# Kernel tuning notes

Measured on AMD Instinct MI355X. Metric: run time of the kernel, lower is better.

The kernel has to match this reference:

```python
import jax, jax.numpy as jnp
import numpy as np

N_NODES = 50000
N_EDGES = 800000
IN_CH = 256
OUT_CH = 64
HEADS = 4
NEG_SLOPE = 0.2


def setup_inputs() -> dict:
    key = jax.random.key(0)
    k = jax.random.split(key, 7)
    x = jax.random.normal(k[0], (N_NODES, IN_CH), dtype=jnp.float32)
    edge_index = jax.random.randint(k[1], (2, N_EDGES), 0, N_NODES, dtype=jnp.int32)
    # Glorot-style init for the linear projection and attention vectors
    W = jax.random.normal(k[2], (IN_CH, HEADS * OUT_CH), dtype=jnp.float32) / np.sqrt(IN_CH)
    att_src = jax.random.normal(k[3], (HEADS, OUT_CH), dtype=jnp.float32) / np.sqrt(OUT_CH)
    att_dst = jax.random.normal(k[4], (HEADS, OUT_CH), dtype=jnp.float32) / np.sqrt(OUT_CH)
    bias = jnp.zeros((HEADS * OUT_CH,), dtype=jnp.float32)
    return {"x": x, "edge_index": edge_index, "W": W,
            "att_src": att_src, "att_dst": att_dst, "bias": bias}


def reference(x, edge_index, W, att_src, att_dst, bias):
    N = x.shape[0]
    # PyG GATConv default: add self-loops
    loop = jnp.arange(N, dtype=edge_index.dtype)
    src = jnp.concatenate([edge_index[0], loop])
    dst = jnp.concatenate([edge_index[1], loop])

    h = (x @ W).reshape(N, HEADS, OUT_CH)          # [N,H,C]
    a_src = jnp.einsum('nhc,hc->nh', h, att_src)    # [N,H]
    a_dst = jnp.einsum('nhc,hc->nh', h, att_dst)    # [N,H]

    alpha = a_src[src] + a_dst[dst]                 # [E,H]
    alpha = jax.nn.leaky_relu(alpha, NEG_SLOPE)

    # segment softmax over edges grouped by destination node
    amax = jax.ops.segment_max(alpha, dst, num_segments=N)
    amax = jnp.where(jnp.isfinite(amax), amax, 0.0)
    e = jnp.exp(alpha - amax[dst])
    denom = jax.ops.segment_sum(e, dst, num_segments=N)
    coef = e / (denom[dst] + 1e-16)                 # [E,H]

    msg = coef[..., None] * h[src]                  # [E,H,C]
    out = jax.ops.segment_sum(msg, dst, num_segments=N)  # [N,H,C]
    out = out.reshape(N, HEADS * OUT_CH) + bias
    return jax.nn.relu(out)
```

## Files before the change

### kernel.cpp

```cpp
#include <hip/hip_runtime.h>
#include <hip/hip_bf16.h>

#define HC 256
#define NEG_SLOPE 0.2f
#define BM 64
#define LDKF 264

typedef short short8_t __attribute__((ext_vector_type(8)));
typedef float float4_t __attribute__((ext_vector_type(4)));
typedef int   int4_t   __attribute__((ext_vector_type(4)));

__device__ __forceinline__ unsigned short f2bf(float f) {
  unsigned u = __float_as_uint(f);
  return (unsigned short)((u + 0x7fffu + ((u >> 16) & 1u)) >> 16);
}
__device__ __forceinline__ float bf2f(unsigned short b) {
  return __uint_as_float(((unsigned)b) << 16);
}

__global__ __launch_bounds__(256) void wq_kernel(
    const float* __restrict__ W, unsigned short* __restrict__ Wq,
    int* __restrict__ deg, int n)
{
  const int f = blockIdx.x * 256 + threadIdx.x;
  if (f < 8192) {
    const int wv    = f >> 11;
    const int nt    = (f >> 9) & 3;
    const int kstep = (f >> 6) & 7;
    const int l     = f & 63;
    const int ncol  = 64 * wv + 16 * nt + (l & 15);
    const int k0    = kstep * 32 + (l >> 4) * 8;
    unsigned pk[4];
    #pragma unroll
    for (int i = 0; i < 4; ++i) {
      __hip_bfloat162 b2 = __float22bfloat162_rn(make_float2(
          W[(k0 + 2 * i) * 256 + ncol], W[(k0 + 2 * i + 1) * 256 + ncol]));
      pk[i] = *(unsigned*)&b2;
    }
    *(uint4*)&Wq[(size_t)f * 8] = make_uint4(pk[0], pk[1], pk[2], pk[3]);
  }
  if (f < n) deg[f] = 0;
}

__global__ __launch_bounds__(256) void gemm_deg(
    const float* __restrict__ x, const unsigned short* __restrict__ Wq,
    const float* __restrict__ att_src, const float* __restrict__ att_dst,
    unsigned short* __restrict__ h, float* __restrict__ a_src,
    float* __restrict__ a_dst, int nnodes,
    const int* __restrict__ ei, int* __restrict__ deg, int E, int NG, int ND)
{
  __shared__ unsigned short As[BM * LDKF];
  const int t = threadIdx.x;

  if (blockIdx.x >= NG) {
    const int b = blockIdx.x - NG;
    for (int e = b * 256 + t; e < E; e += ND * 256)
      atomicAdd(&deg[ei[E + e]], 1);
    return;
  }

  const int wv   = t >> 6;
  const int lane = t & 63;
  const int r0   = blockIdx.x * BM;

  {
    const int row = t >> 2, kcb = (t & 3) * 16;
    const int gr = r0 + row;
    #pragma unroll
    for (int k0 = 0; k0 < 256; k0 += 64) {
      float4 xv[4];
      if (gr < nnodes) {
        const float4* p = (const float4*)(x + (size_t)gr * 256 + k0 + kcb);
        xv[0] = p[0]; xv[1] = p[1]; xv[2] = p[2]; xv[3] = p[3];
      } else {
        xv[0] = xv[1] = xv[2] = xv[3] = make_float4(0.f, 0.f, 0.f, 0.f);
      }
      const float* f = (const float*)xv;
      unsigned pk[8];
      #pragma unroll
      for (int i = 0; i < 8; ++i) {
        __hip_bfloat162 b2 = __float22bfloat162_rn(make_float2(f[2 * i], f[2 * i + 1]));
        pk[i] = *(unsigned*)&b2;
      }
      uint4* d = (uint4*)&As[row * LDKF + k0 + kcb];
      d[0] = make_uint4(pk[0], pk[1], pk[2], pk[3]);
      d[1] = make_uint4(pk[4], pk[5], pk[6], pk[7]);
    }
  }
  __syncthreads();

  const int l15 = lane & 15, q = lane >> 4;
  float4_t acc[4][4] = {};

  const unsigned short* __restrict__ Bq = Wq + (size_t)wv * 16384 + lane * 8;

  #pragma unroll
  for (int kstep = 0; kstep < 8; ++kstep) {
    const int ko = kstep * 32;
    short8_t bfr[4], af[4];
    #pragma unroll
    for (int nt = 0; nt < 4; ++nt)
      bfr[nt] = *(const short8_t*)(Bq + nt * 4096 + kstep * 512);
    #pragma unroll
    for (int mt = 0; mt < 4; ++mt)
      af[mt] = *(const short8_t*)&As[(16 * mt + l15) * LDKF + ko + q * 8];
    #pragma unroll
    for (int mt = 0; mt < 4; ++mt)
      #pragma unroll
      for (int nt = 0; nt < 4; ++nt)
        acc[mt][nt] = __builtin_amdgcn_mfma_f32_16x16x32_bf16(
            bfr[nt], af[mt], acc[mt][nt], 0, 0, 0);
  }

  float4 as4[4], ad4[4];
  #pragma unroll
  for (int nt = 0; nt < 4; ++nt) {
    as4[nt] = *(const float4*)&att_src[64 * wv + 16 * nt + 4 * q];
    ad4[nt] = *(const float4*)&att_dst[64 * wv + 16 * nt + 4 * q];
  }

  #pragma unroll
  for (int mt = 0; mt < 4; ++mt) {
    const int node = r0 + 16 * mt + l15;
    const bool ok = node < nnodes;
    float ps = 0.f, pd = 0.f;
    #pragma unroll
    for (int nt = 0; nt < 4; ++nt) {
      const float4_t v = acc[mt][nt];
      if (ok) {
        __hip_bfloat162 b01 = __float22bfloat162_rn(make_float2(v[0], v[1]));
        __hip_bfloat162 b23 = __float22bfloat162_rn(make_float2(v[2], v[3]));
        uint2 u = make_uint2(*(unsigned*)&b01, *(unsigned*)&b23);
        *(uint2*)&h[(size_t)node * 256 + 64 * wv + 16 * nt + 4 * q] = u;
      }
      ps += v[0] * as4[nt].x + v[1] * as4[nt].y + v[2] * as4[nt].z + v[3] * as4[nt].w;
      pd += v[0] * ad4[nt].x + v[1] * ad4[nt].y + v[2] * ad4[nt].z + v[3] * ad4[nt].w;
    }
    ps += __shfl_down(ps, 16); ps += __shfl_down(ps, 32);
    pd += __shfl_down(pd, 16); pd += __shfl_down(pd, 32);
    if (ok && lane < 16) {
      a_src[node * 4 + wv] = ps;
      a_dst[node * 4 + wv] = pd;
    }
  }
}

__global__ __launch_bounds__(256) void scan_p1(const int* __restrict__ deg,
                                               int* __restrict__ bsum, int n)
{
  __shared__ int ws[4];
  const int t = threadIdx.x, lane = t & 63, wv = t >> 6;
  const int base = blockIdx.x * 1024 + t * 4;
  int4 v = make_int4(0, 0, 0, 0);
  if (base + 3 < n) v = *(const int4*)&deg[base];
  else {
    if (base + 0 < n) v.x = deg[base + 0];
    if (base + 1 < n) v.y = deg[base + 1];
    if (base + 2 < n) v.z = deg[base + 2];
  }
  int s = (v.x + v.y) + (v.z + v.w);
  #pragma unroll
  for (int off = 32; off; off >>= 1) s += __shfl_down(s, off, 64);
  if (lane == 0) ws[wv] = s;
  __syncthreads();
  if (t == 0) bsum[blockIdx.x] = (ws[0] + ws[1]) + (ws[2] + ws[3]);
}

__global__ __launch_bounds__(1024) void scan_p2(const int* __restrict__ bsum,
                                                int* __restrict__ boff,
                                                int* __restrict__ rowptr,
                                                int nb, int n)
{
  __shared__ int wsum[16], woff[16];
  const int t = threadIdx.x, lane = t & 63, wv = t >> 6;
  int v = (t < nb) ? bsum[t] : 0;
  int sc = v;
  #pragma unroll
  for (int off = 1; off < 64; off <<= 1) {
    int u = __shfl_up(sc, off, 64);
    if (lane >= off) sc += u;
  }
  if (lane == 63) wsum[wv] = sc;
  __syncthreads();
  if (t == 0) {
    int run = 0;
    #pragma unroll
    for (int i = 0; i < 16; ++i) { int x = wsum[i]; woff[i] = run; run += x; }
    rowptr[n] = run;
  }
  __syncthreads();
  if (t < nb) boff[t] = woff[wv] + sc - v;
}

__global__ __launch_bounds__(256) void scan_p3(const int* __restrict__ deg,
                                               const int* __restrict__ boff,
                                               int* __restrict__ rowptr,
                                               int* __restrict__ cursor, int n)
{
  __shared__ int wsum[4], woff[4];
  const int t = threadIdx.x, lane = t & 63, wv = t >> 6;
  const int base = blockIdx.x * 1024 + t * 4;
  int4 v = make_int4(0, 0, 0, 0);
  if (base + 3 < n) v = *(const int4*)&deg[base];
  else {
    if (base + 0 < n) v.x = deg[base + 0];
    if (base + 1 < n) v.y = deg[base + 1];
    if (base + 2 < n) v.z = deg[base + 2];
  }
  const int s = (v.x + v.y) + (v.z + v.w);
  int sc = s;
  #pragma unroll
  for (int off = 1; off < 64; off <<= 1) {
    int u = __shfl_up(sc, off, 64);
    if (lane >= off) sc += u;
  }
  if (lane == 63) wsum[wv] = sc;
  __syncthreads();
  if (t == 0) {
    int run = 0;
    #pragma unroll
    for (int i = 0; i < 4; ++i) { int x = wsum[i]; woff[i] = run; run += x; }
  }
  __syncthreads();
  int excl = boff[blockIdx.x] + woff[wv] + (sc - s);
  int4 r;
  r.x = excl;
  r.y = r.x + v.x;
  r.z = r.y + v.y;
  r.w = r.z + v.z;
  if (base + 3 < n) {
    *(int4*)&rowptr[base] = r;
    *(int4*)&cursor[base] = r;
  } else {
    if (base + 0 < n) { rowptr[base + 0] = r.x; cursor[base + 0] = r.x; }
    if (base + 1 < n) { rowptr[base + 1] = r.y; cursor[base + 1] = r.y; }
    if (base + 2 < n) { rowptr[base + 2] = r.z; cursor[base + 2] = r.z; }
  }
}

__global__ __launch_bounds__(256) void fill_csr(
    const int* __restrict__ ei, int* __restrict__ cursor,
    int* __restrict__ csr_src, int E, int nnodes)
{
  const int g    = blockIdx.x & 7;
  const int bg   = blockIdx.x >> 3;
  const int nbg  = gridDim.x >> 3;
  const int gsz  = (nnodes + 7) >> 3;
  const int dlo  = g * gsz;
  const int dhi  = min(dlo + gsz, nnodes);

  for (int e = bg * 256 + threadIdx.x; e < E; e += nbg * 256) {
    const int d = ei[E + e];
    if (d < dlo || d >= dhi) continue;
    const int pos = atomicAdd(&cursor[d], 1);
    csr_src[pos] = ei[e];
  }
}

__device__ __forceinline__ float4 ld_h(const unsigned short* __restrict__ h,
                                       int row, int cb)
{
  const ushort4 u = *(const ushort4*)&h[(size_t)row * 256 + cb];
  return make_float4(bf2f(u.x), bf2f(u.y), bf2f(u.z), bf2f(u.w));
}

__device__ __forceinline__ float edge_w(float as, float ad)
{
  float al = as + ad;
  al = al > 0.f ? al : NEG_SLOPE * al;
  return expf(al);
}

__global__ __launch_bounds__(256) void gather_kernel(
    const int* __restrict__ rowptr, const int* __restrict__ csr_src,
    const unsigned short* __restrict__ h,
    const float* __restrict__ a_src, const float* __restrict__ a_dst,
    const float* __restrict__ bias, float* __restrict__ out, int n)
{
  const int wave = threadIdx.x >> 6;
  const int lane = threadIdx.x & 63;
  const int d = blockIdx.x * 4 + wave;
  if (d >= n) return;

  const int head = lane >> 4;
  const int cb   = lane * 4;

  const float ad = a_dst[d * 4 + head];

  const float w = edge_w(a_src[d * 4 + head], ad);
  float dsum = w;
  float4 hv = ld_h(h, d, cb);
  float4 acc = make_float4(w * hv.x, w * hv.y, w * hv.z, w * hv.w);

  int j = rowptr[d];
  const int end = rowptr[d + 1];

  int4_t sC = {0, 0, 0, 0};
  if (j + 3 < end)
    sC = __builtin_nontemporal_load((const int4_t*)&csr_src[j]);
  while (j + 3 < end) {
    const int jn = j + 4;
    const int jp = (jn + 3 < end) ? jn : j;
    const int4_t sN = __builtin_nontemporal_load((const int4_t*)&csr_src[jp]);

    const float as0 = a_src[sC.x * 4 + head];
    const float as1 = a_src[sC.y * 4 + head];
    const float as2 = a_src[sC.z * 4 + head];
    const float as3 = a_src[sC.w * 4 + head];
    const float4 h0 = ld_h(h, sC.x, cb);
    const float4 h1 = ld_h(h, sC.y, cb);
    const float4 h2 = ld_h(h, sC.z, cb);
    const float4 h3 = ld_h(h, sC.w, cb);

    const float w0 = edge_w(as0, ad);
    const float w1 = edge_w(as1, ad);
    const float w2 = edge_w(as2, ad);
    const float w3 = edge_w(as3, ad);

    dsum += (w0 + w1) + (w2 + w3);
    acc.x += w0 * h0.x + w1 * h1.x + w2 * h2.x + w3 * h3.x;
    acc.y += w0 * h0.y + w1 * h1.y + w2 * h2.y + w3 * h3.y;
    acc.z += w0 * h0.z + w1 * h1.z + w2 * h2.z + w3 * h3.z;
    acc.w += w0 * h0.w + w1 * h1.w + w2 * h2.w + w3 * h3.w;

    sC = sN; j = jn;
  }
  for (; j < end; ++j) {
    const int s0 = csr_src[j];
    const float w0 = edge_w(a_src[s0 * 4 + head], ad);
    const float4 h0 = ld_h(h, s0, cb);
    dsum += w0;
    acc.x += w0 * h0.x; acc.y += w0 * h0.y;
    acc.z += w0 * h0.z; acc.w += w0 * h0.w;
  }

  const float inv = 1.f / (dsum + 1e-16f);
  const float4 b4 = ((const float4*)bias)[lane];
  float4 o;
  o.x = acc.x * inv + b4.x; o.x = o.x > 0.f ? o.x : 0.f;
  o.y = acc.y * inv + b4.y; o.y = o.y > 0.f ? o.y : 0.f;
  o.z = acc.z * inv + b4.z; o.z = o.z > 0.f ? o.z : 0.f;
  o.w = acc.w * inv + b4.w; o.w = o.w > 0.f ? o.w : 0.f;
  *(float4*)&out[(size_t)d * 256 + cb] = o;
}

extern "C" void kernel_launch(void* const* d_in, const int* in_sizes, int n_in,
                              void* d_out, int out_size, void* d_ws, size_t ws_size,
                              hipStream_t stream)
{
  const float* x       = (const float*)d_in[0];
  const int*   ei      = (const int*)d_in[1];
  const float* W       = (const float*)d_in[2];
  const float* att_src = (const float*)d_in[3];
  const float* att_dst = (const float*)d_in[4];
  const float* bias    = (const float*)d_in[5];

  const int nnodes = in_sizes[0] / HC;
  const int E      = in_sizes[1] / 2;
  const int nb     = (nnodes + 1023) / 1024;

  float* out = (float*)d_out;
  char* ws = (char*)d_ws;
  unsigned short* h  = (unsigned short*)ws;
  float* a_src = (float*)(ws + (size_t)nnodes * HC * 2);
  float* a_dst = a_src + (size_t)nnodes * 4;
  unsigned short* Wq = (unsigned short*)(a_dst + (size_t)nnodes * 4);
  int* deg    = (int*)((char*)Wq + 256 * 256 * 2);
  int* rowptr = deg + nnodes;
  int* cursor = rowptr + ((nnodes + 1 + 3) & ~3);
  int* bsum   = cursor + nnodes;
  int* boff   = bsum + ((nb + 3) & ~3);
  int* csr    = boff + ((nb + 3) & ~3);

  const int NG = (nnodes + BM - 1) / BM;
  const int ND = 1024;

  wq_kernel<<<256, 256, 0, stream>>>(W, Wq, deg, nnodes);

  gemm_deg<<<NG + ND, 256, 0, stream>>>(
      x, Wq, att_src, att_dst, h, a_src, a_dst, nnodes, ei, deg, E, NG, ND);

  scan_p1<<<nb, 256, 0, stream>>>(deg, bsum, nnodes);
  scan_p2<<<1, 1024, 0, stream>>>(bsum, boff, rowptr, nb, nnodes);
  scan_p3<<<nb, 256, 0, stream>>>(deg, boff, rowptr, cursor, nnodes);

  fill_csr<<<1024, 256, 0, stream>>>(ei, cursor, csr, E, nnodes);

  gather_kernel<<<(nnodes + 3) / 4, 256, 0, stream>>>(
      rowptr, csr, h, a_src, a_dst, bias, out, nnodes);
}
```

Baseline: 258.9 us.

## Move degree histogram ahead of GEMM and fuse CSR fill into GEMM launch

The degree histogram now runs as its own dst-partitioned kernel before the scan, and the CSR fill blocks are packed into the GEMM launch, so the fill overlaps the projection GEMM instead of the histogram. The gather is also split into two launches covering each half of the nodes. This is meant to hide the atomic-heavy CSR fill behind GEMM work, at the price of leaving the histogram exposed. The gather split adds an extra launch, with no clear benefit since both halves run on the same stream.

```diff
diff --git a/kernel.cpp b/kernel.cpp
--- a/kernel.cpp
+++ b/kernel.cpp
@@ -42,20 +42,141 @@
   if (f < n) deg[f] = 0;
 }
 
-__global__ __launch_bounds__(256) void gemm_deg(
+__global__ __launch_bounds__(256) void hist_kernel(
+    const int* __restrict__ ei, int* __restrict__ deg, int E, int nnodes)
+{
+  const int g    = blockIdx.x & 7;
+  const int bg   = blockIdx.x >> 3;
+  const int nbg  = gridDim.x >> 3;
+  const int gsz  = (nnodes + 7) >> 3;
+  const int dlo  = g * gsz;
+  const int dhi  = min(dlo + gsz, nnodes);
+
+  for (int e = bg * 256 + threadIdx.x; e < E; e += nbg * 256) {
+    const int d = ei[E + e];
+    if (d < dlo || d >= dhi) continue;
+    atomicAdd(&deg[d], 1);
+  }
+}
+
+__global__ __launch_bounds__(256) void scan_p1(const int* __restrict__ deg,
+                                               int* __restrict__ bsum, int n)
+{
+  __shared__ int ws[4];
+  const int t = threadIdx.x, lane = t & 63, wv = t >> 6;
+  const int base = blockIdx.x * 1024 + t * 4;
+  int4 v = make_int4(0, 0, 0, 0);
+  if (base + 3 < n) v = *(const int4*)&deg[base];
+  else {
+    if (base + 0 < n) v.x = deg[base + 0];
+    if (base + 1 < n) v.y = deg[base + 1];
+    if (base + 2 < n) v.z = deg[base + 2];
+  }
+  int s = (v.x + v.y) + (v.z + v.w);
+  #pragma unroll
+  for (int off = 32; off; off >>= 1) s += __shfl_down(s, off, 64);
+  if (lane == 0) ws[wv] = s;
+  __syncthreads();
+  if (t == 0) bsum[blockIdx.x] = (ws[0] + ws[1]) + (ws[2] + ws[3]);
+}
+
+__global__ __launch_bounds__(1024) void scan_p2(const int* __restrict__ bsum,
+                                                int* __restrict__ boff,
+                                                int* __restrict__ rowptr,
+                                                int nb, int n)
+{
+  __shared__ int wsum[16], woff[16];
+  const int t = threadIdx.x, lane = t & 63, wv = t >> 6;
+  int v = (t < nb) ? bsum[t] : 0;
+  int sc = v;
+  #pragma unroll
+  for (int off = 1; off < 64; off <<= 1) {
+    int u = __shfl_up(sc, off, 64);
+    if (lane >= off) sc += u;
+  }
+  if (lane == 63) wsum[wv] = sc;
+  __syncthreads();
+  if (t == 0) {
+    int run = 0;
+    #pragma unroll
+    for (int i = 0; i < 16; ++i) { int x = wsum[i]; woff[i] = run; run += x; }
+    rowptr[n] = run;
+  }
+  __syncthreads();
+  if (t < nb) boff[t] = woff[wv] + sc - v;
+}
+
+__global__ __launch_bounds__(256) void scan_p3(const int* __restrict__ deg,
+                                               const int* __restrict__ boff,
+                                               int* __restrict__ rowptr,
+                                               int* __restrict__ cursor, int n)
+{
+  __shared__ int wsum[4], woff[4];
+  const int t = threadIdx.x, lane = t & 63, wv = t >> 6;
+  const int base = blockIdx.x * 1024 + t * 4;
+  int4 v = make_int4(0, 0, 0, 0);
+  if (base + 3 < n) v = *(const int4*)&deg[base];
+  else {
+    if (base + 0 < n) v.x = deg[base + 0];
+    if (base + 1 < n) v.y = deg[base + 1];
+    if (base + 2 < n) v.z = deg[base + 2];
+  }
+  const int s = (v.x + v.y) + (v.z + v.w);
+  int sc = s;
+  #pragma unroll
+  for (int off = 1; off < 64; off <<= 1) {
+    int u = __shfl_up(sc, off, 64);
+    if (lane >= off) sc += u;
+  }
+  if (lane == 63) wsum[wv] = sc;
+  __syncthreads();
+  if (t == 0) {
+    int run = 0;
+    #pragma unroll
+    for (int i = 0; i < 4; ++i) { int x = wsum[i]; woff[i] = run; run += x; }
+  }
+  __syncthreads();
+  int excl = boff[blockIdx.x] + woff[wv] + (sc - s);
+  int4 r;
+  r.x = excl;
+  r.y = r.x + v.x;
+  r.z = r.y + v.y;
+  r.w = r.z + v.z;
+  if (base + 3 < n) {
+    *(int4*)&rowptr[base] = r;
+    *(int4*)&cursor[base] = r;
+  } else {
+    if (base + 0 < n) { rowptr[base + 0] = r.x; cursor[base + 0] = r.x; }
+    if (base + 1 < n) { rowptr[base + 1] = r.y; cursor[base + 1] = r.y; }
+    if (base + 2 < n) { rowptr[base + 2] = r.z; cursor[base + 2] = r.z; }
+  }
+}
+
+__global__ __launch_bounds__(256) void gemm_fill(
     const float* __restrict__ x, const unsigned short* __restrict__ Wq,
     const float* __restrict__ att_src, const float* __restrict__ att_dst,
     unsigned short* __restrict__ h, float* __restrict__ a_src,
     float* __restrict__ a_dst, int nnodes,
-    const int* __restrict__ ei, int* __restrict__ deg, int E, int NG, int ND)
+    const int* __restrict__ ei, int* __restrict__ cursor,
+    int* __restrict__ csr_src, int E, int NG, int NF)
 {
   __shared__ unsigned short As[BM * LDKF];
   const int t = threadIdx.x;
 
   if (blockIdx.x >= NG) {
-    const int b = blockIdx.x - NG;
-    for (int e = b * 256 + t; e < E; e += ND * 256)
-      atomicAdd(&deg[ei[E + e]], 1);
+    const int b    = blockIdx.x - NG;
+    const int g    = b & 7;
+    const int bg   = b >> 3;
+    const int nbg  = NF >> 3;
+    const int gsz  = (nnodes + 7) >> 3;
+    const int dlo  = g * gsz;
+    const int dhi  = min(dlo + gsz, nnodes);
+    for (int e = bg * 256 + t; e < E; e += nbg * 256) {
+      const int d = ei[E + e];
+      if (d < dlo || d >= dhi) continue;
+      const int pos = atomicAdd(&cursor[d], 1);
+      csr_src[pos] = ei[e];
+    }
     return;
   }
 
@@ -145,118 +266,6 @@
   }
 }
 
-__global__ __launch_bounds__(256) void scan_p1(const int* __restrict__ deg,
-                                               int* __restrict__ bsum, int n)
-{
-  __shared__ int ws[4];
-  const int t = threadIdx.x, lane = t & 63, wv = t >> 6;
-  const int base = blockIdx.x * 1024 + t * 4;
-  int4 v = make_int4(0, 0, 0, 0);
-  if (base + 3 < n) v = *(const int4*)&deg[base];
-  else {
-    if (base + 0 < n) v.x = deg[base + 0];
-    if (base + 1 < n) v.y = deg[base + 1];
-    if (base + 2 < n) v.z = deg[base + 2];
-  }
-  int s = (v.x + v.y) + (v.z + v.w);
-  #pragma unroll
-  for (int off = 32; off; off >>= 1) s += __shfl_down(s, off, 64);
-  if (lane == 0) ws[wv] = s;
-  __syncthreads();
-  if (t == 0) bsum[blockIdx.x] = (ws[0] + ws[1]) + (ws[2] + ws[3]);
-}
-
-__global__ __launch_bounds__(1024) void scan_p2(const int* __restrict__ bsum,
-                                                int* __restrict__ boff,
-                                                int* __restrict__ rowptr,
-                                                int nb, int n)
-{
-  __shared__ int wsum[16], woff[16];
-  const int t = threadIdx.x, lane = t & 63, wv = t >> 6;
-  int v = (t < nb) ? bsum[t] : 0;
-  int sc = v;
-  #pragma unroll
-  for (int off = 1; off < 64; off <<= 1) {
-    int u = __shfl_up(sc, off, 64);
-    if (lane >= off) sc += u;
-  }
-  if (lane == 63) wsum[wv] = sc;
-  __syncthreads();
-  if (t == 0) {
-    int run = 0;
-    #pragma unroll
-    for (int i = 0; i < 16; ++i) { int x = wsum[i]; woff[i] = run; run += x; }
-    rowptr[n] = run;
-  }
-  __syncthreads();
-  if (t < nb) boff[t] = woff[wv] + sc - v;
-}
-
-__global__ __launch_bounds__(256) void scan_p3(const int* __restrict__ deg,
-                                               const int* __restrict__ boff,
-                                               int* __restrict__ rowptr,
-                                               int* __restrict__ cursor, int n)
-{
-  __shared__ int wsum[4], woff[4];
-  const int t = threadIdx.x, lane = t & 63, wv = t >> 6;
-  const int base = blockIdx.x * 1024 + t * 4;
-  int4 v = make_int4(0, 0, 0, 0);
-  if (base + 3 < n) v = *(const int4*)&deg[base];
-  else {
-    if (base + 0 < n) v.x = deg[base + 0];
-    if (base + 1 < n) v.y = deg[base + 1];
-    if (base + 2 < n) v.z = deg[base + 2];
-  }
-  const int s = (v.x + v.y) + (v.z + v.w);
-  int sc = s;
-  #pragma unroll
-  for (int off = 1; off < 64; off <<= 1) {
-    int u = __shfl_up(sc, off, 64);
-    if (lane >= off) sc += u;
-  }
-  if (lane == 63) wsum[wv] = sc;
-  __syncthreads();
-  if (t == 0) {
-    int run = 0;
-    #pragma unroll
-    for (int i = 0; i < 4; ++i) { int x = wsum[i]; woff[i] = run; run += x; }
-  }
-  __syncthreads();
-  int excl = boff[blockIdx.x] + woff[wv] + (sc - s);
-  int4 r;
-  r.x = excl;
-  r.y = r.x + v.x;
-  r.z = r.y + v.y;
-  r.w = r.z + v.z;
-  if (base + 3 < n) {
-    *(int4*)&rowptr[base] = r;
-    *(int4*)&cursor[base] = r;
-  } else {
-    if (base + 0 < n) { rowptr[base + 0] = r.x; cursor[base + 0] = r.x; }
-    if (base + 1 < n) { rowptr[base + 1] = r.y; cursor[base + 1] = r.y; }
-    if (base + 2 < n) { rowptr[base + 2] = r.z; cursor[base + 2] = r.z; }
-  }
-}
-
-__global__ __launch_bounds__(256) void fill_csr(
-    const int* __restrict__ ei, int* __restrict__ cursor,
-    int* __restrict__ csr_src, int E, int nnodes)
-{
-  const int g    = blockIdx.x & 7;
-  const int bg   = blockIdx.x >> 3;
-  const int nbg  = gridDim.x >> 3;
-  const int gsz  = (nnodes + 7) >> 3;
-  const int dlo  = g * gsz;
-  const int dhi  = min(dlo + gsz, nnodes);
-
-  for (int e = bg * 256 + threadIdx.x; e < E; e += nbg * 256) {
-    const int d = ei[E + e];
-    if (d < dlo || d >= dhi) continue;
-    const int pos = atomicAdd(&cursor[d], 1);
-    csr_src[pos] = ei[e];
-  }
-}
-
 __device__ __forceinline__ float4 ld_h(const unsigned short* __restrict__ h,
                                        int row, int cb)
 {
@@ -275,12 +284,12 @@
     const int* __restrict__ rowptr, const int* __restrict__ csr_src,
     const unsigned short* __restrict__ h,
     const float* __restrict__ a_src, const float* __restrict__ a_dst,
-    const float* __restrict__ bias, float* __restrict__ out, int n)
+    const float* __restrict__ bias, float* __restrict__ out, int d0, int dend)
 {
   const int wave = threadIdx.x >> 6;
   const int lane = threadIdx.x & 63;
-  const int d = blockIdx.x * 4 + wave;
-  if (d >= n) return;
+  const int d = d0 + blockIdx.x * 4 + wave;
+  if (d >= dend) return;
 
   const int head = lane >> 4;
   const int cb   = lane * 4;
@@ -373,19 +382,23 @@
   int* csr    = boff + ((nb + 3) & ~3);
 
   const int NG = (nnodes + BM - 1) / BM;
-  const int ND = 1024;
+  const int NF = 1024;
 
   wq_kernel<<<256, 256, 0, stream>>>(W, Wq, deg, nnodes);
 
-  gemm_deg<<<NG + ND, 256, 0, stream>>>(
-      x, Wq, att_src, att_dst, h, a_src, a_dst, nnodes, ei, deg, E, NG, ND);
+  hist_kernel<<<1024, 256, 0, stream>>>(ei, deg, E, nnodes);
 
   scan_p1<<<nb, 256, 0, stream>>>(deg, bsum, nnodes);
   scan_p2<<<1, 1024, 0, stream>>>(bsum, boff, rowptr, nb, nnodes);
   scan_p3<<<nb, 256, 0, stream>>>(deg, boff, rowptr, cursor, nnodes);
 
-  fill_csr<<<1024, 256, 0, stream>>>(ei, cursor, csr, E, nnodes);
-
-  gather_kernel<<<(nnodes + 3) / 4, 256, 0, stream>>>(
-      rowptr, csr, h, a_src, a_dst, bias, out, nnodes);
-}
+  gemm_fill<<<NG + NF, 256, 0, stream>>>(
+      x, Wq, att_src, att_dst, h, a_src, a_dst, nnodes,
+      ei, cursor, csr, E, NG, NF);
+
+  const int half = (nnodes + 1) / 2;
+  gather_kernel<<<(half + 3) / 4, 256, 0, stream>>>(
+      rowptr, csr, h, a_src, a_dst, bias, out, 0, half);
+  gather_kernel<<<(nnodes - half + 3) / 4, 256, 0, stream>>>(
+      rowptr, csr, h, a_src, a_dst, bias, out, half, nnodes);
+}
```

Result: slower. 272.5 us (+5.2%).

## Restructure GEMM to per-wave 16-row tiles reading x directly, split degree count

Applied to the files above, without the earlier changes.

The GEMM no longer stages a 64-row x tile in shared memory. Each wave now owns 16 nodes and all 256 output columns, loading x straight from global memory into MFMA A-fragments and streaming every W column tile per k-step, with all four head attention sums computed per wave and written as a float4. The Wq layout is reordered to match. The degree-count atomics move out of the fused GEMM launch into their own kernel. This removes the LDS staging and barrier, at the cost of each wave reading the whole bf16 W, holding 64 accumulator registers, and losing the overlap between the GEMM and the degree atomics.

```diff
diff --git a/kernel.cpp b/kernel.cpp
--- a/kernel.cpp
+++ b/kernel.cpp
@@ -3,8 +3,6 @@
 
 #define HC 256
 #define NEG_SLOPE 0.2f
-#define BM 64
-#define LDKF 264
 
 typedef short short8_t __attribute__((ext_vector_type(8)));
 typedef float float4_t __attribute__((ext_vector_type(4)));
@@ -24,11 +22,10 @@
 {
   const int f = blockIdx.x * 256 + threadIdx.x;
   if (f < 8192) {
-    const int wv    = f >> 11;
-    const int nt    = (f >> 9) & 3;
+    const int ct    = f >> 9;
     const int kstep = (f >> 6) & 7;
     const int l     = f & 63;
-    const int ncol  = 64 * wv + 16 * nt + (l & 15);
+    const int ncol  = 16 * ct + (l & 15);
     const int k0    = kstep * 32 + (l >> 4) * 8;
     unsigned pk[4];
     #pragma unroll
@@ -42,107 +39,75 @@
   if (f < n) deg[f] = 0;
 }
 
-__global__ __launch_bounds__(256) void gemm_deg(
+__global__ __launch_bounds__(256) void gemm_kernel(
     const float* __restrict__ x, const unsigned short* __restrict__ Wq,
     const float* __restrict__ att_src, const float* __restrict__ att_dst,
     unsigned short* __restrict__ h, float* __restrict__ a_src,
-    float* __restrict__ a_dst, int nnodes,
-    const int* __restrict__ ei, int* __restrict__ deg, int E, int NG, int ND)
-{
-  __shared__ unsigned short As[BM * LDKF];
-  const int t = threadIdx.x;
-
-  if (blockIdx.x >= NG) {
-    const int b = blockIdx.x - NG;
-    for (int e = b * 256 + t; e < E; e += ND * 256)
-      atomicAdd(&deg[ei[E + e]], 1);
-    return;
-  }
-
+    float* __restrict__ a_dst, int nnodes)
+{
+  const int t    = threadIdx.x;
   const int wv   = t >> 6;
   const int lane = t & 63;
-  const int r0   = blockIdx.x * BM;
-
-  {
-    const int row = t >> 2, kcb = (t & 3) * 16;
-    const int gr = r0 + row;
+  const int l15  = lane & 15, q = lane >> 4;
+  const int node = blockIdx.x * 64 + 16 * wv + l15;
+  const bool ok  = node < nnodes;
+  const int nc   = ok ? node : (nnodes - 1);
+  const float* __restrict__ xrow = x + (size_t)nc * 256 + q * 8;
+
+  float4_t acc[16] = {};
+
+  #pragma unroll
+  for (int kstep = 0; kstep < 8; ++kstep) {
+    const float4 xa = *(const float4*)(xrow + kstep * 32);
+    const float4 xb = *(const float4*)(xrow + kstep * 32 + 4);
+    __hip_bfloat162 c0 = __float22bfloat162_rn(make_float2(xa.x, xa.y));
+    __hip_bfloat162 c1 = __float22bfloat162_rn(make_float2(xa.z, xa.w));
+    __hip_bfloat162 c2 = __float22bfloat162_rn(make_float2(xb.x, xb.y));
+    __hip_bfloat162 c3 = __float22bfloat162_rn(make_float2(xb.z, xb.w));
+    uint4 pk = make_uint4(*(unsigned*)&c0, *(unsigned*)&c1,
+                          *(unsigned*)&c2, *(unsigned*)&c3);
+    const short8_t af = *(const short8_t*)&pk;
+
+    const unsigned short* __restrict__ Bk = Wq + kstep * 512 + lane * 8;
     #pragma unroll
-    for (int k0 = 0; k0 < 256; k0 += 64) {
-      float4 xv[4];
-      if (gr < nnodes) {
-        const float4* p = (const float4*)(x + (size_t)gr * 256 + k0 + kcb);
-        xv[0] = p[0]; xv[1] = p[1]; xv[2] = p[2]; xv[3] = p[3];
-      } else {
-        xv[0] = xv[1] = xv[2] = xv[3] = make_float4(0.f, 0.f, 0.f, 0.f);
-      }
-      const float* f = (const float*)xv;
-      unsigned pk[8];
-      #pragma unroll
-      for (int i = 0; i < 8; ++i) {
-        __hip_bfloat162 b2 = __float22bfloat162_rn(make_float2(f[2 * i], f[2 * i + 1]));
-        pk[i] = *(unsigned*)&b2;
-      }
-      uint4* d = (uint4*)&As[row * LDKF + k0 + kcb];
-      d[0] = make_uint4(pk[0], pk[1], pk[2], pk[3]);
-      d[1] = make_uint4(pk[4], pk[5], pk[6], pk[7]);
+    for (int ct = 0; ct < 16; ++ct) {
+      const short8_t bfr = *(const short8_t*)(Bk + ct * 4096);
+      acc[ct] = __builtin_amdgcn_mfma_f32_16x16x32_bf16(bfr, af, acc[ct], 0, 0, 0);
     }
   }
-  __syncthreads();
-
-  const int l15 = lane & 15, q = lane >> 4;
-  float4_t acc[4][4] = {};
-
-  const unsigned short* __restrict__ Bq = Wq + (size_t)wv * 16384 + lane * 8;
-
-  #pragma unroll
-  for (int kstep = 0; kstep < 8; ++kstep) {
-    const int ko = kstep * 32;
-    short8_t bfr[4], af[4];
-    #pragma unroll
-    for (int nt = 0; nt < 4; ++nt)
-      bfr[nt] = *(const short8_t*)(Bq + nt * 4096 + kstep * 512);
-    #pragma unroll
-    for (int mt = 0; mt < 4; ++mt)
-      af[mt] = *(const short8_t*)&As[(16 * mt + l15) * LDKF + ko + q * 8];
-    #pragma unroll
-    for (int mt = 0; mt < 4; ++mt)
-      #pragma unroll
-      for (int nt = 0; nt < 4; ++nt)
-        acc[mt][nt] = __builtin_amdgcn_mfma_f32_16x16x32_bf16(
-            bfr[nt], af[mt], acc[mt][nt], 0, 0, 0);
-  }
-
-  float4 as4[4], ad4[4];
-  #pragma unroll
-  for (int nt = 0; nt < 4; ++nt) {
-    as4[nt] = *(const float4*)&att_src[64 * wv + 16 * nt + 4 * q];
-    ad4[nt] = *(const float4*)&att_dst[64 * wv + 16 * nt + 4 * q];
-  }
-
-  #pragma unroll
-  for (int mt = 0; mt < 4; ++mt) {
-    const int node = r0 + 16 * mt + l15;
-    const bool ok = node < nnodes;
-    float ps = 0.f, pd = 0.f;
-    #pragma unroll
-    for (int nt = 0; nt < 4; ++nt) {
-      const float4_t v = acc[mt][nt];
-      if (ok) {
-        __hip_bfloat162 b01 = __float22bfloat162_rn(make_float2(v[0], v[1]));
-        __hip_bfloat162 b23 = __float22bfloat162_rn(make_float2(v[2], v[3]));
-        uint2 u = make_uint2(*(unsigned*)&b01, *(unsigned*)&b23);
-        *(uint2*)&h[(size_t)node * 256 + 64 * wv + 16 * nt + 4 * q] = u;
-      }
-      ps += v[0] * as4[nt].x + v[1] * as4[nt].y + v[2] * as4[nt].z + v[3] * as4[nt].w;
-      pd += v[0] * ad4[nt].x + v[1] * ad4[nt].y + v[2] * ad4[nt].z + v[3] * ad4[nt].w;
+
+  float ps[4] = {0.f, 0.f, 0.f, 0.f}, pd[4] = {0.f, 0.f, 0.f, 0.f};
+  #pragma unroll
+  for (int ct = 0; ct < 16; ++ct) {
+    const float4_t v = acc[ct];
+    if (ok) {
+      __hip_bfloat162 b01 = __float22bfloat162_rn(make_float2(v[0], v[1]));
+      __hip_bfloat162 b23 = __float22bfloat162_rn(make_float2(v[2], v[3]));
+      uint2 u = make_uint2(*(unsigned*)&b01, *(unsigned*)&b23);
+      *(uint2*)&h[(size_t)node * 256 + 16 * ct + 4 * q] = u;
     }
-    ps += __shfl_down(ps, 16); ps += __shfl_down(ps, 32);
-    pd += __shfl_down(pd, 16); pd += __shfl_down(pd, 32);
-    if (ok && lane < 16) {
-      a_src[node * 4 + wv] = ps;
-      a_dst[node * 4 + wv] = pd;
-    }
-  }
+    const float4 as4 = *(const float4*)&att_src[16 * ct + 4 * q];
+    const float4 ad4 = *(const float4*)&att_dst[16 * ct + 4 * q];
+    const int hh = ct >> 2;
+    ps[hh] += v[0] * as4.x + v[1] * as4.y + v[2] * as4.z + v[3] * as4.w;
+    pd[hh] += v[0] * ad4.x + v[1] * ad4.y + v[2] * ad4.z + v[3] * ad4.w;
+  }
+  #pragma unroll
+  for (int hh = 0; hh < 4; ++hh) {
+    ps[hh] += __shfl_down(ps[hh], 16); ps[hh] += __shfl_down(ps[hh], 32);
+    pd[hh] += __shfl_down(pd[hh], 16); pd[hh] += __shfl_down(pd[hh], 32);
+  }
+  if (ok && lane < 16) {
+    *(float4*)&a_src[node * 4] = make_float4(ps[0], ps[1], ps[2], ps[3]);
+    *(float4*)&a_dst[node * 4] = make_float4(pd[0], pd[1], pd[2], pd[3]);
+  }
+}
+
+__global__ void deg_count(const int* __restrict__ ei, int* __restrict__ deg, int E)
+{
+  const int e = blockIdx.x * blockDim.x + threadIdx.x;
+  if (e >= E) return;
+  atomicAdd(&deg[ei[E + e]], 1);
 }
 
 __global__ __launch_bounds__(256) void scan_p1(const int* __restrict__ deg,
@@ -372,13 +337,12 @@
   int* boff   = bsum + ((nb + 3) & ~3);
   int* csr    = boff + ((nb + 3) & ~3);
 
-  const int NG = (nnodes + BM - 1) / BM;
-  const int ND = 1024;
-
   wq_kernel<<<256, 256, 0, stream>>>(W, Wq, deg, nnodes);
 
-  gemm_deg<<<NG + ND, 256, 0, stream>>>(
-      x, Wq, att_src, att_dst, h, a_src, a_dst, nnodes, ei, deg, E, NG, ND);
+  gemm_kernel<<<(nnodes + 63) / 64, 256, 0, stream>>>(
+      x, Wq, att_src, att_dst, h, a_src, a_dst, nnodes);
+
+  deg_count<<<(E + 255) / 256, 256, 0, stream>>>(ei, deg, E);
 
   scan_p1<<<nb, 256, 0, stream>>>(deg, bsum, nnodes);
   scan_p2<<<1, 1024, 0, stream>>>(bsum, boff, rowptr, nb, nnodes);
```

After: 351.9 us. 35.9% more time.
